# Optimization experiments

Measured on AMD Instinct MI355X. Metric: run time of the kernel, lower is better.

## Reference

```python
import jax, jax.numpy as jnp
import numpy as np

B, S, D, H = 2, 2048, 1024, 16
HD = D // H  # 64

def setup_inputs() -> dict:
    key = jax.random.key(0)
    ks = jax.random.split(key, 11)
    s = 1.0 / np.sqrt(D)
    inp = {
        "q": jax.random.normal(ks[0], (B, S, D), jnp.float32),
        "k": jax.random.normal(ks[1], (B, S, D), jnp.float32),
        "v": jax.random.normal(ks[2], (B, S, D), jnp.float32),
        "Wq": jax.random.normal(ks[3], (D, D), jnp.float32) * s,
        "bq": jnp.zeros((D,), jnp.float32),
        "Wk": jax.random.normal(ks[4], (D, D), jnp.float32) * s,
        "bk": jnp.zeros((D,), jnp.float32),
        "Wv": jax.random.normal(ks[5], (D, D), jnp.float32) * s,
        "bv": jnp.zeros((D,), jnp.float32),
        "Wo": jax.random.normal(ks[6], (D, D), jnp.float32) * s,
        "bo": jnp.zeros((D,), jnp.float32),
    }
    return inp

def _split_heads(x):
    # [B,S,D] -> [B,H,S,HD]
    b = x.shape[0]
    return x.reshape(b, -1, H, HD).transpose(0, 2, 1, 3)

def reference(q, k, v, Wq, bq, Wk, bk, Wv, bv, Wo, bo):
    qh = _split_heads(q @ Wq.T + bq)
    kh = _split_heads(k @ Wk.T + bk)
    vh = _split_heads(v @ Wv.T + bv)
    scale = 1.0 / jnp.sqrt(jnp.asarray(HD, qh.dtype))
    scores = jnp.einsum("bhqd,bhkd->bhqk", qh, kh) * scale  # [B,H,S,S]
    atten = jax.nn.softmax(scores, axis=-1)  # dropout is eval-mode no-op
    ctx = jnp.einsum("bhqk,bhkd->bhqd", atten, vh)
    out = ctx.transpose(0, 2, 1, 3).reshape(q.shape[0], -1, D)
    return out @ Wo.T + bo, atten
```

## Files before the change

### kernel.cpp

```cpp
#include <hip/hip_runtime.h>
#include <cstdint>

#define B_ 2
#define S_ 2048
#define D_ 1024
#define H_ 16

typedef __bf16 bf16x8 __attribute__((ext_vector_type(8)));
typedef __bf16 bf16x4 __attribute__((ext_vector_type(4)));
typedef float  f32x4  __attribute__((ext_vector_type(4)));

__device__ __forceinline__ void g2l16(const void* g, void* l) {
  auto* gp = reinterpret_cast<const __attribute__((address_space(1))) uint32_t*>(
      reinterpret_cast<uintptr_t>(g));
  auto* lp = reinterpret_cast<__attribute__((address_space(3))) uint32_t*>(
      reinterpret_cast<uintptr_t>(l));
  __builtin_amdgcn_global_load_lds(gp, lp, 16, 0, 0);
}

__device__ __forceinline__ float exp2_hw(float x) {
#if __has_builtin(__builtin_amdgcn_exp2f)
  return __builtin_amdgcn_exp2f(x);
#else
  return __exp2f(x);
#endif
}

struct CvtArgs {
  const float* s[4];
  __bf16* d[4];
};

__global__ __launch_bounds__(256) void k_cvt(CvtArgs a) {
  int t = blockIdx.y;
  long base = ((long)blockIdx.x * blockDim.x + threadIdx.x) * 8;
  const float4* sp = (const float4*)(a.s[t] + base);
  float4 x = sp[0], y = sp[1];
  bf16x8 o;
  o[0] = (__bf16)x.x; o[1] = (__bf16)x.y; o[2] = (__bf16)x.z; o[3] = (__bf16)x.w;
  o[4] = (__bf16)y.x; o[5] = (__bf16)y.y; o[6] = (__bf16)y.z; o[7] = (__bf16)y.w;
  *(bf16x8*)(a.d[t] + base) = o;
}

__global__ __launch_bounds__(256, 3) void k_proj(
    const float* __restrict__ Xq, const float* __restrict__ Xk, const float* __restrict__ Xv,
    const __bf16* __restrict__ Wq, const __bf16* __restrict__ Wk, const __bf16* __restrict__ Wv,
    const float* __restrict__ bq, const float* __restrict__ bk, const float* __restrict__ bv,
    __bf16* __restrict__ Oq, __bf16* __restrict__ Ok, __bf16* __restrict__ OvT)
{
  int o = (blockIdx.x % 96) * 8 + blockIdx.x / 96;
  int nb = o & 7, mb = (o >> 3) & 31, z = o >> 8;

  const float* X = (z == 0) ? Xq : (z == 1) ? Xk : Xv;
  const __bf16* W = (z == 0) ? Wq : (z == 1) ? Wk : Wv;
  const float* bias = (z == 0) ? bq : (z == 1) ? bk : bv;
  float scale = (z == 0) ? 0.180336880111183f : 1.0f;

  __shared__ __align__(16) char smem[40960];
  bf16x8 (*As)[512] = (bf16x8(*)[512])smem;
  bf16x8 (*Bs)[512] = (bf16x8(*)[512])(smem + 16384);

  int t = threadIdx.x, lane = t & 63, w = t >> 6;
  int l15 = lane & 15, l4 = lane >> 4;
  int wr = w >> 1, wc = w & 1;
  int m0 = mb * 128, n0 = nb * 128;

  int arow = t >> 1, ac2 = (t & 1) * 2;
  const float* Xs = X + (size_t)(m0 + arow) * 1024 + (t & 1) * 16;
  int srow = t >> 2, sc = t & 3;
  const __bf16* Wsp = W + (size_t)(n0 + srow) * 1024 + sc * 8;
  int ldsoff = __builtin_amdgcn_readfirstlane(w * 1024);

  float4 a0, a1, a2, a3;

#define ALOAD(kt)                                                              \
  {                                                                            \
    const float4* ap = (const float4*)(Xs + (size_t)(kt) * 32);                \
    a0 = ap[0]; a1 = ap[1]; a2 = ap[2]; a3 = ap[3];                            \
  }
#define AWRITE(buf)                                                            \
  {                                                                            \
    bf16x8 lo, hi;                                                             \
    lo[0] = (__bf16)a0.x; lo[1] = (__bf16)a0.y; lo[2] = (__bf16)a0.z;          \
    lo[3] = (__bf16)a0.w; lo[4] = (__bf16)a1.x; lo[5] = (__bf16)a1.y;          \
    lo[6] = (__bf16)a1.z; lo[7] = (__bf16)a1.w;                                \
    hi[0] = (__bf16)a2.x; hi[1] = (__bf16)a2.y; hi[2] = (__bf16)a2.z;          \
    hi[3] = (__bf16)a2.w; hi[4] = (__bf16)a3.x; hi[5] = (__bf16)a3.y;          \
    hi[6] = (__bf16)a3.z; hi[7] = (__bf16)a3.w;                                \
    As[buf][arow * 4 + ac2] = lo;                                              \
    As[buf][arow * 4 + ac2 + 1] = hi;                                          \
  }
#define BSTG(buf, kt)                                                          \
  {                                                                            \
    _Pragma("unroll")                                                          \
    for (int i = 0; i < 2; ++i) {                                              \
      int lo_ = __builtin_amdgcn_readfirstlane(i * 4096 + ldsoff);             \
      g2l16(Wsp + (size_t)i * 64 * 1024 + (kt) * 32, (char*)Bs[buf] + lo_);    \
    }                                                                          \
  }

  f32x4 acc[4][4] = {};

  BSTG(0, 0)
  ALOAD(0)
  BSTG(1, 1)
  asm volatile("s_waitcnt vmcnt(2)" ::: "memory");
  AWRITE(0)
  ALOAD(1)
  asm volatile("s_waitcnt lgkmcnt(0)" ::: "memory");
  __builtin_amdgcn_s_barrier();
  __builtin_amdgcn_sched_barrier(0);

  int bring = 0;
  for (int kt = 0; kt < 32; ++kt) {
    int bcur = bring;
    int bp2 = (bring >= 1) ? bring - 1 : 2;
    int acur = kt & 1, anxt = acur ^ 1;
    if (kt + 2 < 32) BSTG(bp2, kt + 2)
    __builtin_amdgcn_sched_barrier(0);

    bf16x8 af[4], bfr[4];
#pragma unroll
    for (int i = 0; i < 4; ++i) af[i] = As[acur][(wr * 64 + i * 16 + l15) * 4 + l4];
#pragma unroll
    for (int j = 0; j < 4; ++j) bfr[j] = Bs[bcur][(wc * 64 + j * 16 + l15) * 4 + l4];
#pragma unroll
    for (int i = 0; i < 4; ++i)
#pragma unroll
      for (int j = 0; j < 4; ++j)
        acc[i][j] = __builtin_amdgcn_mfma_f32_16x16x32_bf16(af[i], bfr[j], acc[i][j], 0, 0, 0);
    __builtin_amdgcn_sched_barrier(0);

    if (kt + 1 < 32) {
      if (kt + 2 < 32) {
        asm volatile("s_waitcnt vmcnt(2)" ::: "memory");
      } else {
        asm volatile("s_waitcnt vmcnt(0)" ::: "memory");
      }
      AWRITE(anxt)
      if (kt + 2 < 32) ALOAD(kt + 2)
      asm volatile("s_waitcnt lgkmcnt(0)" ::: "memory");
      __builtin_amdgcn_s_barrier();
      __builtin_amdgcn_sched_barrier(0);
    }
    bring = (bring == 2) ? 0 : bring + 1;
  }
#undef ALOAD
#undef AWRITE
#undef BSTG

  if (z == 2) {
    __syncthreads();
    __bf16* Tt = (__bf16*)smem;
    const int LDT = 136;
    int b = m0 >> 11, ss0 = m0 & 2047;
#pragma unroll
    for (int p = 0; p < 2; ++p) {
      if (wc == p) {
#pragma unroll
        for (int j = 0; j < 4; ++j) {
          float bv_ = bias[n0 + p * 64 + j * 16 + l15];
#pragma unroll
          for (int i = 0; i < 4; ++i) {
            bf16x4 pv;
#pragma unroll
            for (int r = 0; r < 4; ++r) pv[r] = (__bf16)(acc[i][j][r] + bv_);
            *(bf16x4*)&Tt[(j * 16 + l15) * LDT + wr * 64 + i * 16 + l4 * 4] = pv;
          }
        }
      }
      __syncthreads();
      int h = (n0 >> 6) + p;
      __bf16* dst = OvT + ((size_t)(b * H_ + h) * 64) * S_ + ss0;
#pragma unroll
      for (int it = 0; it < 4; ++it) {
        int nl = it * 16 + (t >> 4);
        int mc = (t & 15) * 8;
        bf16x8 vv = *(bf16x8*)&Tt[nl * LDT + mc];
        *(bf16x8*)(dst + (size_t)nl * S_ + mc) = vv;
      }
      __syncthreads();
    }
  } else {
    __bf16* O = (z == 0) ? Oq : Ok;
#pragma unroll
    for (int j = 0; j < 4; ++j) {
      int col = n0 + wc * 64 + j * 16 + l15;
      float bv_ = bias[col];
      int h = col >> 6, hd = col & 63;
#pragma unroll
      for (int i = 0; i < 4; ++i) {
#pragma unroll
        for (int r = 0; r < 4; ++r) {
          int row = m0 + wr * 64 + i * 16 + l4 * 4 + r;
          int b = row >> 11, ss = row & 2047;
          float val = (acc[i][j][r] + bv_) * scale;
          O[(((size_t)b * H_ + h) * S_ + ss) * 64 + hd] = (__bf16)val;
        }
      }
    }
  }
}

__global__ __launch_bounds__(512, 4) void k_attn(
    const __bf16* __restrict__ Qh, const __bf16* __restrict__ Kh,
    const __bf16* __restrict__ VhT, float* __restrict__ atten,
    __bf16* __restrict__ ctxb)
{
  __shared__ bf16x8 KVl[3][1024];
  __shared__ bf16x8 Pl[8 * 176];

  int bid = blockIdx.x;
  int sb = (bid & 7) * 64 + (bid >> 3);
  int bh = sb >> 4, qt = sb & 15;
  int t = threadIdx.x, lane = t & 63, w = t >> 6;
  int l15 = lane & 15, l4 = lane >> 4;
  int q0 = qt * 128 + w * 16;

  const __bf16* Qp = Qh + ((size_t)bh * S_ + q0) * 64;
  bf16x8 qf0 = *(const bf16x8*)(Qp + (size_t)l15 * 64 + l4 * 8);
  bf16x8 qf1 = *(const bf16x8*)(Qp + (size_t)l15 * 64 + 32 + l4 * 8);

  int srow = t >> 3, sc8 = t & 7;
  int scs = sc8 ^ (srow & 7);
  int wbase = __builtin_amdgcn_readfirstlane(w * 1024);

  const __bf16* KpS = Kh + (size_t)bh * S_ * 64 + (size_t)srow * 64 + scs * 8;
  const __bf16* VpS = VhT + (size_t)bh * 64 * S_ + (size_t)srow * S_ + scs * 8;

  float l_part[4] = {0.f, 0.f, 0.f, 0.f};

#define ASTAGE(buf, kt)                                                        \
  {                                                                            \
    g2l16(KpS + (size_t)(kt) * 8192, (char*)KVl[buf] + wbase);                 \
    g2l16(KpS + (size_t)(kt) * 8192 + 4096, (char*)KVl[buf] + 8192 + wbase);   \
  }

  ASTAGE(0, 0)
  ASTAGE(1, 1)
  asm volatile("s_waitcnt vmcnt(2)" ::: "memory");
  __builtin_amdgcn_s_barrier();
  __builtin_amdgcn_sched_barrier(0);

  {
    int ring = 0;
    for (int kt = 0; kt < 16; ++kt) {
      int cur = ring;
      int rp2 = (ring == 0) ? 2 : ring - 1;
      if (kt + 2 < 16) ASTAGE(rp2, kt + 2)
      __builtin_amdgcn_sched_barrier(0);

#pragma unroll
      for (int t8 = 0; t8 < 8; ++t8) {
        int kr = t8 * 16 + l15;
        bf16x8 kf0 = KVl[cur][kr * 8 + ((l4) ^ (kr & 7))];
        bf16x8 kf1 = KVl[cur][kr * 8 + ((4 + l4) ^ (kr & 7))];
        f32x4 a_ = {0.f, 0.f, 0.f, 0.f};
        a_ = __builtin_amdgcn_mfma_f32_16x16x32_bf16(qf0, kf0, a_, 0, 0, 0);
        a_ = __builtin_amdgcn_mfma_f32_16x16x32_bf16(qf1, kf1, a_, 0, 0, 0);
#pragma unroll
        for (int r = 0; r < 4; ++r) l_part[r] += exp2_hw(a_[r]);
      }

      if (kt < 14) {
        asm volatile("s_waitcnt vmcnt(2)" ::: "memory");
        __builtin_amdgcn_s_barrier();
        __builtin_amdgcn_sched_barrier(0);
      } else if (kt == 14) {
        asm volatile("s_waitcnt vmcnt(0)" ::: "memory");
        __builtin_amdgcn_s_barrier();
        __builtin_amdgcn_sched_barrier(0);
      }
      ring = (ring == 2) ? 0 : ring + 1;
    }
  }
#undef ASTAGE

  float inv_l[4];
#pragma unroll
  for (int r = 0; r < 4; ++r) {
    float l = l_part[r];
    l += __shfl_xor(l, 1);
    l += __shfl_xor(l, 2);
    l += __shfl_xor(l, 4);
    l += __shfl_xor(l, 8);
    inv_l[r] = 1.0f / l;
  }

  __builtin_amdgcn_s_barrier();
  __builtin_amdgcn_sched_barrier(0);

  f32x4 ctx[4] = {};
  float* aRow = atten + ((size_t)bh * S_ + q0) * S_;
  __bf16* PlW = (__bf16*)(Pl + w * 176);

#define BSTAGE(buf, kt)                                                        \
  {                                                                            \
    g2l16(KpS + (size_t)(kt) * 4096, (char*)KVl[buf] + wbase);                 \
    g2l16(VpS + (size_t)(kt) * 64, (char*)KVl[buf] + 8192 + wbase);            \
  }

  BSTAGE(0, 0)
  BSTAGE(1, 1)
  asm volatile("s_waitcnt vmcnt(2)" ::: "memory");
  __builtin_amdgcn_s_barrier();
  __builtin_amdgcn_sched_barrier(0);

  {
    int ring = 0;
    for (int kt = 0; kt < 32; ++kt) {
      int cur = ring;
      int rp2 = (ring == 0) ? 2 : ring - 1;
      if (kt + 2 < 32) BSTAGE(rp2, kt + 2)
      __builtin_amdgcn_sched_barrier(0);

      f32x4 sc[4];
#pragma unroll
      for (int t8 = 0; t8 < 4; ++t8) {
        int kr = t8 * 16 + l15;
        bf16x8 kf0 = KVl[cur][kr * 8 + ((l4) ^ (kr & 7))];
        bf16x8 kf1 = KVl[cur][kr * 8 + ((4 + l4) ^ (kr & 7))];
        f32x4 a_ = {0.f, 0.f, 0.f, 0.f};
        a_ = __builtin_amdgcn_mfma_f32_16x16x32_bf16(qf0, kf0, a_, 0, 0, 0);
        a_ = __builtin_amdgcn_mfma_f32_16x16x32_bf16(qf1, kf1, a_, 0, 0, 0);
        sc[t8] = a_;
      }

#pragma unroll
      for (int t8 = 0; t8 < 4; ++t8) {
#pragma unroll
        for (int r = 0; r < 4; ++r) {
          float p = exp2_hw(sc[t8][r]) * inv_l[r];
          aRow[(size_t)(l4 * 4 + r) * S_ + kt * 64 + t8 * 16 + l15] = p;
          PlW[(l4 * 4 + r) * 88 + t8 * 16 + l15] = (__bf16)p;
        }
      }

#pragma unroll
      for (int kc = 0; kc < 2; ++kc) {
        bf16x8 pa = Pl[w * 176 + l15 * 11 + kc * 4 + l4];
#pragma unroll
        for (int dt = 0; dt < 4; ++dt) {
          int vr = dt * 16 + l15;
          bf16x8 vf = KVl[cur][512 + vr * 8 + ((kc * 4 + l4) ^ (vr & 7))];
          ctx[dt] = __builtin_amdgcn_mfma_f32_16x16x32_bf16(pa, vf, ctx[dt], 0, 0, 0);
        }
      }

      if (kt < 31) {
        asm volatile("s_waitcnt vmcnt(18)" ::: "memory");
        __builtin_amdgcn_s_barrier();
        __builtin_amdgcn_sched_barrier(0);
      }
      ring = (ring == 2) ? 0 : ring + 1;
    }
  }
#undef BSTAGE

  int b = bh >> 4, h = bh & 15;
#pragma unroll
  for (int dt = 0; dt < 4; ++dt) {
#pragma unroll
    for (int r = 0; r < 4; ++r) {
      size_t row = (size_t)b * S_ + q0 + l4 * 4 + r;
      ctxb[row * D_ + h * 64 + dt * 16 + l15] = (__bf16)ctx[dt][r];
    }
  }
}

__global__ __launch_bounds__(256, 3) void k_out(
    const __bf16* __restrict__ X, const __bf16* __restrict__ W,
    const float* __restrict__ bias, float* __restrict__ O)
{
  __shared__ bf16x8 As[3][512];
  __shared__ bf16x8 Bs[3][512];

  int o = (blockIdx.x % 32) * 8 + blockIdx.x / 32;
  int nb = o & 7, mb = o >> 3;

  int t = threadIdx.x, lane = t & 63, w = t >> 6;
  int l15 = lane & 15, l4 = lane >> 4;
  int wr = w >> 1, wc = w & 1;
  int m0 = mb * 128, n0 = nb * 128;

  int srow = t >> 2, sc = t & 3;
  int ldsoff = __builtin_amdgcn_readfirstlane(w * 1024);
  const __bf16* Xs = X + (size_t)(m0 + srow) * 1024 + sc * 8;
  const __bf16* Wsp = W + (size_t)(n0 + srow) * 1024 + sc * 8;

#define PSTAGE(buf, kt)                                                        \
  {                                                                            \
    _Pragma("unroll")                                                          \
    for (int i = 0; i < 2; ++i) {                                              \
      int lo = __builtin_amdgcn_readfirstlane(i * 4096 + ldsoff);              \
      g2l16(Xs + (size_t)i * 64 * 1024 + (kt) * 32, (char*)As[buf] + lo);      \
      g2l16(Wsp + (size_t)i * 64 * 1024 + (kt) * 32, (char*)Bs[buf] + lo);     \
    }                                                                          \
  }

  f32x4 acc[4][4] = {};

  PSTAGE(0, 0)
  PSTAGE(1, 1)
  asm volatile("s_waitcnt vmcnt(4)" ::: "memory");
  __builtin_amdgcn_s_barrier();
  __builtin_amdgcn_sched_barrier(0);

  int ring = 0;
  for (int kt = 0; kt < 32; ++kt) {
    int cur = ring;
    int rp2 = (ring == 0) ? 2 : ring - 1;
    if (kt + 2 < 32) PSTAGE(rp2, kt + 2)
    __builtin_amdgcn_sched_barrier(0);

    bf16x8 af[4], bfr[4];
#pragma unroll
    for (int i = 0; i < 4; ++i) af[i] = As[cur][(wr * 64 + i * 16 + l15) * 4 + l4];
#pragma unroll
    for (int j = 0; j < 4; ++j) bfr[j] = Bs[cur][(wc * 64 + j * 16 + l15) * 4 + l4];
#pragma unroll
    for (int i = 0; i < 4; ++i)
#pragma unroll
      for (int j = 0; j < 4; ++j)
        acc[i][j] = __builtin_amdgcn_mfma_f32_16x16x32_bf16(af[i], bfr[j], acc[i][j], 0, 0, 0);

    if (kt < 30) {
      asm volatile("s_waitcnt vmcnt(4)" ::: "memory");
      __builtin_amdgcn_s_barrier();
      __builtin_amdgcn_sched_barrier(0);
    } else if (kt == 30) {
      asm volatile("s_waitcnt vmcnt(0)" ::: "memory");
      __builtin_amdgcn_s_barrier();
      __builtin_amdgcn_sched_barrier(0);
    }
    ring = (ring == 2) ? 0 : ring + 1;
  }
#undef PSTAGE

#pragma unroll
  for (int j = 0; j < 4; ++j) {
    int col = n0 + wc * 64 + j * 16 + l15;
    float bv_ = bias[col];
#pragma unroll
    for (int i = 0; i < 4; ++i) {
#pragma unroll
      for (int r = 0; r < 4; ++r) {
        int row = m0 + wr * 64 + i * 16 + l4 * 4 + r;
        O[(size_t)row * 1024 + col] = acc[i][j][r] + bv_;
      }
    }
  }
}

extern "C" void kernel_launch(void* const* d_in, const int* in_sizes, int n_in,
                              void* d_out, int out_size, void* d_ws, size_t ws_size,
                              hipStream_t stream)
{
  const float* q  = (const float*)d_in[0];
  const float* k  = (const float*)d_in[1];
  const float* v  = (const float*)d_in[2];
  const float* Wq = (const float*)d_in[3];
  const float* bq = (const float*)d_in[4];
  const float* Wk = (const float*)d_in[5];
  const float* bk = (const float*)d_in[6];
  const float* Wv = (const float*)d_in[7];
  const float* bv = (const float*)d_in[8];
  const float* Wo = (const float*)d_in[9];
  const float* bo = (const float*)d_in[10];

  const size_t NBSD = (size_t)B_ * S_ * D_;
  const size_t NDD  = (size_t)D_ * D_;

  float* out = (float*)d_out;
  float* atten = out + NBSD;

  if (ws_size < (4 * NDD + 4 * NBSD) * 2) return;

  __bf16* ws = (__bf16*)d_ws;
  __bf16* Wqb = ws;
  __bf16* Wkb = Wqb + NDD;
  __bf16* Wvb = Wkb + NDD;
  __bf16* Wob = Wvb + NDD;
  __bf16* Qh  = Wob + NDD;
  __bf16* Kh  = Qh + NBSD;
  __bf16* VhT = Kh + NBSD;
  __bf16* ctxb = VhT + NBSD;

  CvtArgs ca;
  ca.s[0] = Wq; ca.d[0] = Wqb;
  ca.s[1] = Wk; ca.d[1] = Wkb;
  ca.s[2] = Wv; ca.d[2] = Wvb;
  ca.s[3] = Wo; ca.d[3] = Wob;

  k_cvt<<<dim3(512, 4), 256, 0, stream>>>(ca);
  k_proj<<<dim3(768), 256, 0, stream>>>(q, k, v, Wqb, Wkb, Wvb,
                                        bq, bk, bv, Qh, Kh, VhT);
  k_attn<<<dim3(512), 512, 0, stream>>>(Qh, Kh, VhT, atten, ctxb);
  k_out<<<dim3(256), 256, 0, stream>>>(ctxb, Wob, bo, out);
}
```

Baseline: 239.0 us.

## Double attention block to 1024 threads covering 256 query rows per block

```diff
diff --git a/kernel.cpp b/kernel.cpp
--- a/kernel.cpp
+++ b/kernel.cpp
@@ -202,43 +202,46 @@
   }
 }
 
-__global__ __launch_bounds__(512, 4) void k_attn(
+__global__ __launch_bounds__(1024, 1) void k_attn(
     const __bf16* __restrict__ Qh, const __bf16* __restrict__ Kh,
     const __bf16* __restrict__ VhT, float* __restrict__ atten,
     __bf16* __restrict__ ctxb)
 {
   __shared__ bf16x8 KVl[3][1024];
-  __shared__ bf16x8 Pl[8 * 176];
+  __shared__ bf16x8 Pl[16 * 176];
 
   int bid = blockIdx.x;
-  int sb = (bid & 7) * 64 + (bid >> 3);
-  int bh = sb >> 4, qt = sb & 15;
+  int sb = (bid & 7) * 32 + (bid >> 3);
+  int bh = sb >> 3, qt = sb & 7;
   int t = threadIdx.x, lane = t & 63, w = t >> 6;
   int l15 = lane & 15, l4 = lane >> 4;
-  int q0 = qt * 128 + w * 16;
+  int q0 = qt * 256 + w * 16;
 
   const __bf16* Qp = Qh + ((size_t)bh * S_ + q0) * 64;
   bf16x8 qf0 = *(const bf16x8*)(Qp + (size_t)l15 * 64 + l4 * 8);
   bf16x8 qf1 = *(const bf16x8*)(Qp + (size_t)l15 * 64 + 32 + l4 * 8);
 
-  int srow = t >> 3, sc8 = t & 7;
-  int scs = sc8 ^ (srow & 7);
   int wbase = __builtin_amdgcn_readfirstlane(w * 1024);
 
-  const __bf16* KpS = Kh + (size_t)bh * S_ * 64 + (size_t)srow * 64 + scs * 8;
-  const __bf16* VpS = VhT + (size_t)bh * 64 * S_ + (size_t)srow * S_ + scs * 8;
+  int r128 = t >> 3, c8 = t & 7;
+  int scsA = c8 ^ (r128 & 7);
+  const __bf16* KpA = Kh + (size_t)bh * S_ * 64 + (size_t)r128 * 64 + scsA * 8;
+
+  int rB = t >> 3;
+  int rr = (rB < 64) ? rB : rB - 64;
+  int scsB = c8 ^ (rr & 7);
+  const __bf16* srcB = (rB < 64)
+      ? (Kh + (size_t)bh * S_ * 64 + (size_t)rr * 64 + scsB * 8)
+      : (VhT + (size_t)bh * 64 * S_ + (size_t)rr * S_ + scsB * 8);
+  size_t stepB = (rB < 64) ? 4096 : 64;
 
   float l_part[4] = {0.f, 0.f, 0.f, 0.f};
 
-#define ASTAGE(buf, kt)                                                        \
-  {                                                                            \
-    g2l16(KpS + (size_t)(kt) * 8192, (char*)KVl[buf] + wbase);                 \
-    g2l16(KpS + (size_t)(kt) * 8192 + 4096, (char*)KVl[buf] + 8192 + wbase);   \
-  }
+#define ASTAGE(buf, kt) g2l16(KpA + (size_t)(kt) * 8192, (char*)KVl[buf] + wbase);
 
   ASTAGE(0, 0)
   ASTAGE(1, 1)
-  asm volatile("s_waitcnt vmcnt(2)" ::: "memory");
+  asm volatile("s_waitcnt vmcnt(1)" ::: "memory");
   __builtin_amdgcn_s_barrier();
   __builtin_amdgcn_sched_barrier(0);
 
@@ -263,7 +266,7 @@
       }
 
       if (kt < 14) {
-        asm volatile("s_waitcnt vmcnt(2)" ::: "memory");
+        asm volatile("s_waitcnt vmcnt(1)" ::: "memory");
         __builtin_amdgcn_s_barrier();
         __builtin_amdgcn_sched_barrier(0);
       } else if (kt == 14) {
@@ -294,15 +297,11 @@
   float* aRow = atten + ((size_t)bh * S_ + q0) * S_;
   __bf16* PlW = (__bf16*)(Pl + w * 176);
 
-#define BSTAGE(buf, kt)                                                        \
-  {                                                                            \
-    g2l16(KpS + (size_t)(kt) * 4096, (char*)KVl[buf] + wbase);                 \
-    g2l16(VpS + (size_t)(kt) * 64, (char*)KVl[buf] + 8192 + wbase);            \
-  }
+#define BSTAGE(buf, kt) g2l16(srcB + (size_t)(kt) * stepB, (char*)KVl[buf] + wbase);
 
   BSTAGE(0, 0)
   BSTAGE(1, 1)
-  asm volatile("s_waitcnt vmcnt(2)" ::: "memory");
+  asm volatile("s_waitcnt vmcnt(1)" ::: "memory");
   __builtin_amdgcn_s_barrier();
   __builtin_amdgcn_sched_barrier(0);
 
@@ -347,8 +346,16 @@
         }
       }
 
-      if (kt < 31) {
-        asm volatile("s_waitcnt vmcnt(18)" ::: "memory");
+      if (kt == 0) {
+        asm volatile("s_waitcnt vmcnt(17)" ::: "memory");
+        __builtin_amdgcn_s_barrier();
+        __builtin_amdgcn_sched_barrier(0);
+      } else if (kt < 30) {
+        asm volatile("s_waitcnt vmcnt(33)" ::: "memory");
+        __builtin_amdgcn_s_barrier();
+        __builtin_amdgcn_sched_barrier(0);
+      } else if (kt == 30) {
+        asm volatile("s_waitcnt vmcnt(32)" ::: "memory");
         __builtin_amdgcn_s_barrier();
         __builtin_amdgcn_sched_barrier(0);
       }
@@ -495,6 +502,6 @@
   k_cvt<<<dim3(512, 4), 256, 0, stream>>>(ca);
   k_proj<<<dim3(768), 256, 0, stream>>>(q, k, v, Wqb, Wkb, Wvb,
                                         bq, bk, bv, Qh, Kh, VhT);
-  k_attn<<<dim3(512), 512, 0, stream>>>(Qh, Kh, VhT, atten, ctxb);
+  k_attn<<<dim3(256), 1024, 0, stream>>>(Qh, Kh, VhT, atten, ctxb);
   k_out<<<dim3(256), 256, 0, stream>>>(ctxb, Wob, bo, out);
 }
```

Result: slower. 277.5 us (+16.1%).

## Transpose score MFMA operands so each lane holds one query row, vectorize stores

Applied to the files above, without the earlier changes.

```diff
diff --git a/kernel.cpp b/kernel.cpp
--- a/kernel.cpp
+++ b/kernel.cpp
@@ -228,7 +228,7 @@
   const __bf16* KpS = Kh + (size_t)bh * S_ * 64 + (size_t)srow * 64 + scs * 8;
   const __bf16* VpS = VhT + (size_t)bh * 64 * S_ + (size_t)srow * S_ + scs * 8;
 
-  float l_part[4] = {0.f, 0.f, 0.f, 0.f};
+  float l_part = 0.f;
 
 #define ASTAGE(buf, kt)                                                        \
   {                                                                            \
@@ -256,10 +256,10 @@
         bf16x8 kf0 = KVl[cur][kr * 8 + ((l4) ^ (kr & 7))];
         bf16x8 kf1 = KVl[cur][kr * 8 + ((4 + l4) ^ (kr & 7))];
         f32x4 a_ = {0.f, 0.f, 0.f, 0.f};
-        a_ = __builtin_amdgcn_mfma_f32_16x16x32_bf16(qf0, kf0, a_, 0, 0, 0);
-        a_ = __builtin_amdgcn_mfma_f32_16x16x32_bf16(qf1, kf1, a_, 0, 0, 0);
-#pragma unroll
-        for (int r = 0; r < 4; ++r) l_part[r] += exp2_hw(a_[r]);
+        a_ = __builtin_amdgcn_mfma_f32_16x16x32_bf16(kf0, qf0, a_, 0, 0, 0);
+        a_ = __builtin_amdgcn_mfma_f32_16x16x32_bf16(kf1, qf1, a_, 0, 0, 0);
+#pragma unroll
+        for (int r = 0; r < 4; ++r) l_part += exp2_hw(a_[r]);
       }
 
       if (kt < 14) {
@@ -276,22 +276,19 @@
   }
 #undef ASTAGE
 
-  float inv_l[4];
-#pragma unroll
-  for (int r = 0; r < 4; ++r) {
-    float l = l_part[r];
-    l += __shfl_xor(l, 1);
-    l += __shfl_xor(l, 2);
-    l += __shfl_xor(l, 4);
-    l += __shfl_xor(l, 8);
-    inv_l[r] = 1.0f / l;
+  float inv_l;
+  {
+    float l = l_part;
+    l += __shfl_xor(l, 16);
+    l += __shfl_xor(l, 32);
+    inv_l = 1.0f / l;
   }
 
   __builtin_amdgcn_s_barrier();
   __builtin_amdgcn_sched_barrier(0);
 
   f32x4 ctx[4] = {};
-  float* aRow = atten + ((size_t)bh * S_ + q0) * S_;
+  float* aRowT = atten + ((size_t)bh * S_ + q0 + l15) * S_;
   __bf16* PlW = (__bf16*)(Pl + w * 176);
 
 #define BSTAGE(buf, kt)                                                        \
@@ -321,19 +318,23 @@
         bf16x8 kf0 = KVl[cur][kr * 8 + ((l4) ^ (kr & 7))];
         bf16x8 kf1 = KVl[cur][kr * 8 + ((4 + l4) ^ (kr & 7))];
         f32x4 a_ = {0.f, 0.f, 0.f, 0.f};
-        a_ = __builtin_amdgcn_mfma_f32_16x16x32_bf16(qf0, kf0, a_, 0, 0, 0);
-        a_ = __builtin_amdgcn_mfma_f32_16x16x32_bf16(qf1, kf1, a_, 0, 0, 0);
+        a_ = __builtin_amdgcn_mfma_f32_16x16x32_bf16(kf0, qf0, a_, 0, 0, 0);
+        a_ = __builtin_amdgcn_mfma_f32_16x16x32_bf16(kf1, qf1, a_, 0, 0, 0);
         sc[t8] = a_;
       }
 
 #pragma unroll
       for (int t8 = 0; t8 < 4; ++t8) {
+        f32x4 pv;
+        bf16x4 pb;
 #pragma unroll
         for (int r = 0; r < 4; ++r) {
-          float p = exp2_hw(sc[t8][r]) * inv_l[r];
-          aRow[(size_t)(l4 * 4 + r) * S_ + kt * 64 + t8 * 16 + l15] = p;
-          PlW[(l4 * 4 + r) * 88 + t8 * 16 + l15] = (__bf16)p;
+          float p = exp2_hw(sc[t8][r]) * inv_l;
+          pv[r] = p;
+          pb[r] = (__bf16)p;
         }
+        *(f32x4*)(aRowT + kt * 64 + t8 * 16 + l4 * 4) = pv;
+        *(bf16x4*)(PlW + l15 * 88 + t8 * 16 + l4 * 4) = pb;
       }
 
 #pragma unroll
@@ -347,8 +348,16 @@
         }
       }
 
-      if (kt < 31) {
-        asm volatile("s_waitcnt vmcnt(18)" ::: "memory");
+      if (kt == 0) {
+        asm volatile("s_waitcnt vmcnt(6)" ::: "memory");
+        __builtin_amdgcn_s_barrier();
+        __builtin_amdgcn_sched_barrier(0);
+      } else if (kt < 30) {
+        asm volatile("s_waitcnt vmcnt(10)" ::: "memory");
+        __builtin_amdgcn_s_barrier();
+        __builtin_amdgcn_sched_barrier(0);
+      } else if (kt == 30) {
+        asm volatile("s_waitcnt vmcnt(8)" ::: "memory");
         __builtin_amdgcn_s_barrier();
         __builtin_amdgcn_sched_barrier(0);
       }
```

Measured after the change: 248.5 us. 4.0% more time.
